# Kernel tuning notes

Measured on AMD Instinct MI355X. Metric: run time of the kernel, lower is better.

Reference implementation:

```python
import jax, jax.numpy as jnp
import numpy as np

N = 100000   # nodes
E = 1600000  # edges (avg degree 16)
F_IN = 128
HID = 128
C_OUT = 10
BN_EPS = 1e-5


def setup_inputs() -> dict:
    key = jax.random.key(0)
    ks = jax.random.split(key, 20)
    x = jax.random.normal(ks[0], (N, F_IN), jnp.float32)
    src = jax.random.randint(ks[1], (E,), 0, N)
    dst = jax.random.randint(ks[2], (E,), 0, N)
    def lin(k, fi, fo):
        return jax.random.normal(k, (fi, fo), jnp.float32) * (1.0 / np.sqrt(fi))
    inp = {
        "x": x, "src": src, "dst": dst,
        "W1": lin(ks[3], F_IN, HID), "b1": jnp.zeros((HID,), jnp.float32),
        "g1": jax.random.normal(ks[4], (HID,), jnp.float32) * 0.1 + 1.0,
        "be1": jax.random.normal(ks[5], (HID,), jnp.float32) * 0.1,
        "m1": jax.random.normal(ks[6], (HID,), jnp.float32) * 0.1,
        "v1": jax.random.uniform(ks[7], (HID,), jnp.float32, 0.5, 1.5),
        "W2": lin(ks[8], HID, HID), "b2": jnp.zeros((HID,), jnp.float32),
        "g2": jax.random.normal(ks[9], (HID,), jnp.float32) * 0.1 + 1.0,
        "be2": jax.random.normal(ks[10], (HID,), jnp.float32) * 0.1,
        "m2": jax.random.normal(ks[11], (HID,), jnp.float32) * 0.1,
        "v2": jax.random.uniform(ks[12], (HID,), jnp.float32, 0.5, 1.5),
        "W3": lin(ks[13], HID, C_OUT), "b3": jnp.zeros((C_OUT,), jnp.float32),
    }
    return inp


def _gcn_conv(x, W, b, src, dst):
    # PyG GCNConv: linear, add self-loops, symmetric deg^-1/2 normalization, scatter-add.
    h = x @ W                                            # [N, out]
    deg = jax.ops.segment_sum(jnp.ones((E,), h.dtype), dst, num_segments=N) + 1.0  # self-loop
    dinv = jax.lax.rsqrt(deg)                            # deg^{-1/2}, [N]
    coef = dinv[src] * dinv[dst]                         # per-edge norm, [E]
    agg = jax.ops.segment_sum(h[src] * coef[:, None], dst, num_segments=N)
    agg = agg + h * (dinv * dinv)[:, None]               # self-loop contribution
    return agg + b


def _bn_eval(x, g, be, m, v):
    return (x - m) * jax.lax.rsqrt(v + BN_EPS) * g + be


def reference(x, src, dst, W1, b1, g1, be1, m1, v1,
              W2, b2, g2, be2, m2, v2, W3, b3):
    h = jax.nn.relu(_bn_eval(_gcn_conv(x, W1, b1, src, dst), g1, be1, m1, v1))
    h = jax.nn.relu(_bn_eval(_gcn_conv(h, W2, b2, src, dst), g2, be2, m2, v2))
    return _gcn_conv(h, W3, b3, src, dst)                # [N, C_OUT] logits
```

## Files before the change

### kernel.cpp

```cpp
#include <hip/hip_runtime.h>

#define NN 100000
#define NE 1600000
#define FD 128
#define CO 10
#define BN_EPS 1e-5f
#define NBUK 782
#define NBUKP 784
#define BCAP 3072
#define SEGE 8192
#define NSEG 196
#define H3P 16

typedef __attribute__((ext_vector_type(8))) short short8;
typedef __attribute__((ext_vector_type(4))) float f32x4;

__device__ __forceinline__ unsigned short f2bf(float f) {
  unsigned int u = __builtin_bit_cast(unsigned int, f);
  u = (u + 0x7FFFu + ((u >> 16) & 1u)) >> 16;
  return (unsigned short)u;
}
__device__ __forceinline__ float bf2f(unsigned short h) {
  unsigned int u = ((unsigned int)h) << 16;
  return __builtin_bit_cast(float, u);
}
__device__ __forceinline__ float blo(unsigned int u) {
  return __builtin_bit_cast(float, u << 16);
}
__device__ __forceinline__ float bhi(unsigned int u) {
  return __builtin_bit_cast(float, u & 0xFFFF0000u);
}
__device__ __forceinline__ unsigned int cvt_pk_bf16(float a, float b) {
  unsigned int r;
  asm("v_cvt_pk_bf16_f32 %0, %1, %2" : "=v"(r) : "v"(a), "v"(b));
  return r;
}

__global__ __launch_bounds__(256) void k_hist_prep(
    const int* __restrict__ dst, int* __restrict__ histM,
    const float* __restrict__ W1, const float* __restrict__ W2,
    unsigned short* __restrict__ w1hi, unsigned short* __restrict__ w1lo,
    unsigned short* __restrict__ w2hi, unsigned short* __restrict__ w2lo,
    const float* __restrict__ b1, const float* __restrict__ g1,
    const float* __restrict__ be1, const float* __restrict__ m1,
    const float* __restrict__ v1,
    const float* __restrict__ b2, const float* __restrict__ g2,
    const float* __restrict__ be2, const float* __restrict__ m2,
    const float* __restrict__ v2,
    float* __restrict__ sc1, float* __restrict__ sh1,
    float* __restrict__ sc2, float* __restrict__ sh2) {
  __shared__ int hist[NBUK];
  int b = blockIdx.x, t = threadIdx.x;
  if (b < NSEG) {
    for (int i = t; i < NBUK; i += 256) hist[i] = 0;
    __syncthreads();
    int e0 = b * SEGE, e1 = min(e0 + SEGE, NE);
    for (int e = e0 + t; e < e1; e += 256) atomicAdd(&hist[dst[e] >> 7], 1);
    __syncthreads();
    for (int i = t; i < NBUK; i += 256) histM[b * NBUKP + i] = hist[i];
  } else if (b < NSEG + 128) {
    int bb = b - NSEG;
    const float* W = (bb < 64) ? W1 : W2;
    unsigned short* whi = (bb < 64) ? w1hi : w2hi;
    unsigned short* wlo = (bb < 64) ? w1lo : w2lo;
    int i = (bb & 63) * 256 + t;
    int k = i >> 7, n = i & 127;
    float w = W[i];
    unsigned short h = f2bf(w);
    unsigned short l = f2bf(w - bf2f(h));
    int idx = ((((k >> 5) * 8) + (n >> 4)) * 64 + ((k >> 3) & 3) * 16 + (n & 15)) * 8 + (k & 7);
    whi[idx] = h;
    wlo[idx] = l;
  } else {
    if (t < FD) {
      float s = g1[t] * rsqrtf(v1[t] + BN_EPS);
      sc1[t] = s;
      sh1[t] = (b1[t] - m1[t]) * s + be1[t];
    } else if (t < 2 * FD) {
      int f = t - FD;
      float s = g2[f] * rsqrtf(v2[f] + BN_EPS);
      sc2[f] = s;
      sh2[f] = (b2[f] - m2[f]) * s + be2[f];
    }
  }
}

__global__ __launch_bounds__(256) void k_colscan(const int* __restrict__ histM,
                                                 int* __restrict__ segbase,
                                                 int* __restrict__ btot) {
  __shared__ int lds[256];
  int b = blockIdx.x, t = threadIdx.x;
  int v = (t < NSEG) ? histM[t * NBUKP + b] : 0;
  lds[t] = v;
  __syncthreads();
  int mine = v;
  for (int off = 1; off < 256; off <<= 1) {
    int add = (t >= off) ? lds[t - off] : 0;
    __syncthreads();
    lds[t] += add;
    __syncthreads();
  }
  if (t < NSEG) segbase[t * NBUKP + b] = lds[t] - mine;
  if (t == 255) btot[b] = lds[255];
}

__global__ __launch_bounds__(256) void k_scatter2(const int* __restrict__ src,
                                                  const int* __restrict__ dst,
                                                  const int* __restrict__ segbase,
                                                  unsigned int* __restrict__ buck) {
  __shared__ int base[NBUK];
  int b = blockIdx.x, t = threadIdx.x;
  for (int i = t; i < NBUK; i += 256) base[i] = segbase[b * NBUKP + i];
  __syncthreads();
  int e0 = b * SEGE, e1 = min(e0 + SEGE, NE);
  for (int e = e0 + t; e < e1; e += 256) {
    int s = src[e], d = dst[e];
    int bk = d >> 7;
    int slot = atomicAdd(&base[bk], 1);
    buck[(size_t)bk * BCAP + slot] = ((unsigned int)(d & 127) << 17) | (unsigned int)s;
  }
}

__global__ __launch_bounds__(256) void k_finalize(const int* __restrict__ btot,
                                                  const unsigned int* __restrict__ buck,
                                                  uint4* __restrict__ nrange,
                                                  int* __restrict__ csr_src) {
  __shared__ unsigned int ebuf[BCAP];
  __shared__ int cnt[128];
  __shared__ int xoff[128];
  int b = blockIdx.x, t = threadIdx.x;
  int nb = btot[b];
  const unsigned int* bp = buck + (size_t)b * BCAP;
  for (int i = t; i < nb; i += 256) ebuf[i] = bp[i];
  if (t < 128) cnt[t] = 0;
  __syncthreads();
  for (int i = t; i < nb; i += 256) atomicAdd(&cnt[ebuf[i] >> 17], 1);
  __syncthreads();
  if (t < 128) xoff[t] = cnt[t];
  __syncthreads();
  for (int off = 1; off < 128; off <<= 1) {
    int add = 0;
    if (t < 128 && t >= off) add = xoff[t - off];
    __syncthreads();
    if (t < 128) xoff[t] += add;
    __syncthreads();
  }
  if (t < 128) {
    int node = b * 128 + t;
    int ex = xoff[t] - cnt[t];
    if (node < NN) {
      uint4 nr;
      nr.x = (unsigned)(b * BCAP + ex);
      nr.y = (unsigned)cnt[t];
      nr.z = __builtin_bit_cast(unsigned int, rsqrtf((float)cnt[t] + 1.0f));
      nr.w = 0;
      nrange[node] = nr;
    }
    xoff[t] = ex;
    cnt[t] = 0;
  }
  __syncthreads();
  int base = b * BCAP;
  for (int i = t; i < nb; i += 256) {
    unsigned int p = ebuf[i];
    int dl = (int)(p >> 17);
    int l = atomicAdd(&cnt[dl], 1);
    csr_src[base + xoff[dl] + l] = (int)(p & 0x1FFFFu);
  }
}

__global__ __launch_bounds__(256) void k_gemm128_mfma(const float* __restrict__ X,
                                                      const unsigned short* __restrict__ whi,
                                                      const unsigned short* __restrict__ wlo,
                                                      const uint4* __restrict__ nrange,
                                                      unsigned short* __restrict__ Hbs,
                                                      int nrows) {
  int tid = threadIdx.x;
  int lane = tid & 63, wv = tid >> 6;
  int lg = lane >> 4, li = lane & 15;
  int wr0 = blockIdx.x * 64 + wv * 16;
  int row = wr0 + li;
  bool ok = row < nrows;

  short8 ahi[4], alo[4];
#pragma unroll
  for (int ks = 0; ks < 4; ++ks) {
    if (ok) {
      const float* xp = X + (unsigned)(row * FD + ks * 32 + lg * 8);
      float4 v0 = *(const float4*)xp;
      float4 v1 = *(const float4*)(xp + 4);
      float f[8] = {v0.x, v0.y, v0.z, v0.w, v1.x, v1.y, v1.z, v1.w};
      unsigned int hp[4], lp[4];
#pragma unroll
      for (int j = 0; j < 4; ++j) {
        float a = f[2 * j], c = f[2 * j + 1];
        hp[j] = cvt_pk_bf16(a, c);
        float ra = a - blo(hp[j]);
        float rc = c - bhi(hp[j]);
        lp[j] = cvt_pk_bf16(ra, rc);
      }
      uint4 hv = {hp[0], hp[1], hp[2], hp[3]};
      uint4 lv = {lp[0], lp[1], lp[2], lp[3]};
      ahi[ks] = __builtin_bit_cast(short8, hv);
      alo[ks] = __builtin_bit_cast(short8, lv);
    } else {
#pragma unroll
      for (int j = 0; j < 8; ++j) { ahi[ks][j] = 0; alo[ks][j] = 0; }
    }
  }

  int rb = wr0 + lg * 4;
  float dvr[4];
#pragma unroll
  for (int r = 0; r < 4; ++r)
    dvr[r] = (rb + r < nrows) ? __builtin_bit_cast(float, nrange[rb + r].z) : 0.f;

#pragma unroll
  for (int nt = 0; nt < 8; ++nt) {
    f32x4 acc = {0.f, 0.f, 0.f, 0.f};
#pragma unroll
    for (int ks = 0; ks < 4; ++ks) {
      unsigned int bidx = (unsigned)(((ks * 8 + nt) * 64 + lane) * 8);
      short8 bh = *(const short8*)&whi[bidx];
      short8 bl = *(const short8*)&wlo[bidx];
      acc = __builtin_amdgcn_mfma_f32_16x16x32_bf16(ahi[ks], bh, acc, 0, 0, 0);
      acc = __builtin_amdgcn_mfma_f32_16x16x32_bf16(alo[ks], bh, acc, 0, 0, 0);
      acc = __builtin_amdgcn_mfma_f32_16x16x32_bf16(ahi[ks], bl, acc, 0, 0, 0);
    }
    int col = nt * 16 + li;
#pragma unroll
    for (int r = 0; r < 4; ++r) {
      if (rb + r < nrows)
        Hbs[(unsigned)((rb + r) * FD + col)] = f2bf(acc[r] * dvr[r]);
    }
  }
}

__global__ __launch_bounds__(256) void k_gemm128_bf16A(const unsigned short* __restrict__ Ab,
                                                       const unsigned short* __restrict__ whi,
                                                       const unsigned short* __restrict__ wlo,
                                                       const uint4* __restrict__ nrange,
                                                       unsigned short* __restrict__ Hbs,
                                                       int nrows) {
  int tid = threadIdx.x;
  int lane = tid & 63, wv = tid >> 6;
  int lg = lane >> 4, li = lane & 15;
  int wr0 = blockIdx.x * 64 + wv * 16;
  int row = wr0 + li;
  bool ok = row < nrows;

  short8 ahi[4];
#pragma unroll
  for (int ks = 0; ks < 4; ++ks) {
    if (ok) {
      ahi[ks] = *(const short8*)(Ab + (unsigned)(row * FD + ks * 32 + lg * 8));
    } else {
#pragma unroll
      for (int j = 0; j < 8; ++j) ahi[ks][j] = 0;
    }
  }

  int rb = wr0 + lg * 4;
  float dvr[4];
#pragma unroll
  for (int r = 0; r < 4; ++r)
    dvr[r] = (rb + r < nrows) ? __builtin_bit_cast(float, nrange[rb + r].z) : 0.f;

#pragma unroll
  for (int nt = 0; nt < 8; ++nt) {
    f32x4 acc = {0.f, 0.f, 0.f, 0.f};
#pragma unroll
    for (int ks = 0; ks < 4; ++ks) {
      unsigned int bidx = (unsigned)(((ks * 8 + nt) * 64 + lane) * 8);
      short8 bh = *(const short8*)&whi[bidx];
      short8 bl = *(const short8*)&wlo[bidx];
      acc = __builtin_amdgcn_mfma_f32_16x16x32_bf16(ahi[ks], bh, acc, 0, 0, 0);
      acc = __builtin_amdgcn_mfma_f32_16x16x32_bf16(ahi[ks], bl, acc, 0, 0, 0);
    }
    int col = nt * 16 + li;
#pragma unroll
    for (int r = 0; r < 4; ++r) {
      if (rb + r < nrows)
        Hbs[(unsigned)((rb + r) * FD + col)] = f2bf(acc[r] * dvr[r]);
    }
  }
}

__global__ __launch_bounds__(256) void k_gather128(const uint4* __restrict__ nrange,
                                                   const int* __restrict__ csr_src,
                                                   const unsigned short* __restrict__ Hbs,
                                                   const float* __restrict__ sc,
                                                   const float* __restrict__ sh,
                                                   unsigned int* __restrict__ AGGb) {
  int node = blockIdx.x * 4 + (threadIdx.x >> 6);
  node = __builtin_amdgcn_readfirstlane(node);
  int lane = threadIdx.x & 63;
  const unsigned int* Hc = (const unsigned int*)Hbs;
  uint4 nr = nrange[node];
  int beg = (int)nr.x, end = (int)(nr.x + nr.y);
  float dv = __builtin_bit_cast(float, nr.z);
  float px0, px1 = 0.f, px2 = 0.f, px3 = 0.f;
  float py0, py1 = 0.f, py2 = 0.f, py3 = 0.f;
  {
    unsigned int us = Hc[(unsigned)(node * 64) + lane];
    px0 = blo(us); py0 = bhi(us);
  }
  int e = beg;
  for (; e + 3 < end; e += 4) {
    unsigned int u0 = Hc[((unsigned)csr_src[e + 0] << 6) + lane];
    unsigned int u1 = Hc[((unsigned)csr_src[e + 1] << 6) + lane];
    unsigned int u2 = Hc[((unsigned)csr_src[e + 2] << 6) + lane];
    unsigned int u3 = Hc[((unsigned)csr_src[e + 3] << 6) + lane];
    px0 += blo(u0); py0 += bhi(u0);
    px1 += blo(u1); py1 += bhi(u1);
    px2 += blo(u2); py2 += bhi(u2);
    px3 += blo(u3); py3 += bhi(u3);
  }
  for (; e < end; ++e) {
    unsigned int u0 = Hc[((unsigned)csr_src[e] << 6) + lane];
    px0 += blo(u0); py0 += bhi(u0);
  }
  float accx = ((px0 + px1) + (px2 + px3)) * dv;
  float accy = ((py0 + py1) + (py2 + py3)) * dv;
  float scx = sc[lane * 2], scy = sc[lane * 2 + 1];
  float shx = sh[lane * 2], shy = sh[lane * 2 + 1];
  accx = fmaxf(fmaf(accx, scx, shx), 0.f);
  accy = fmaxf(fmaf(accy, scy, shy), 0.f);
  AGGb[(unsigned)(node * 64) + lane] = cvt_pk_bf16(accx, accy);
}

__global__ __launch_bounds__(256) void k_gather128_out(const uint4* __restrict__ nrange,
                                                       const int* __restrict__ csr_src,
                                                       const unsigned short* __restrict__ Hbs,
                                                       const float* __restrict__ sc,
                                                       const float* __restrict__ sh,
                                                       const float* __restrict__ W3,
                                                       float* __restrict__ H3s) {
  int node = blockIdx.x * 4 + (threadIdx.x >> 6);
  node = __builtin_amdgcn_readfirstlane(node);
  int lane = threadIdx.x & 63;
  float w3r[20];
  {
    const float* wp = W3 + lane * 2 * CO;
#pragma unroll
    for (int j = 0; j < 20; ++j) w3r[j] = wp[j];
  }
  const unsigned int* Hc = (const unsigned int*)Hbs;
  uint4 nr = nrange[node];
  int beg = (int)nr.x, end = (int)(nr.x + nr.y);
  float dv = __builtin_bit_cast(float, nr.z);
  float px0, px1 = 0.f, px2 = 0.f, px3 = 0.f;
  float py0, py1 = 0.f, py2 = 0.f, py3 = 0.f;
  {
    unsigned int us = Hc[(unsigned)(node * 64) + lane];
    px0 = blo(us); py0 = bhi(us);
  }
  int e = beg;
  for (; e + 3 < end; e += 4) {
    unsigned int u0 = Hc[((unsigned)csr_src[e + 0] << 6) + lane];
    unsigned int u1 = Hc[((unsigned)csr_src[e + 1] << 6) + lane];
    unsigned int u2 = Hc[((unsigned)csr_src[e + 2] << 6) + lane];
    unsigned int u3 = Hc[((unsigned)csr_src[e + 3] << 6) + lane];
    px0 += blo(u0); py0 += bhi(u0);
    px1 += blo(u1); py1 += bhi(u1);
    px2 += blo(u2); py2 += bhi(u2);
    px3 += blo(u3); py3 += bhi(u3);
  }
  for (; e < end; ++e) {
    unsigned int u0 = Hc[((unsigned)csr_src[e] << 6) + lane];
    px0 += blo(u0); py0 += bhi(u0);
  }
  float accx = ((px0 + px1) + (px2 + px3)) * dv;
  float accy = ((py0 + py1) + (py2 + py3)) * dv;
  float scx = sc[lane * 2], scy = sc[lane * 2 + 1];
  float shx = sh[lane * 2], shy = sh[lane * 2 + 1];
  accx = fmaxf(fmaf(accx, scx, shx), 0.f);
  accy = fmaxf(fmaf(accy, scy, shy), 0.f);
  float p[10];
#pragma unroll
  for (int c = 0; c < CO; ++c) p[c] = fmaf(accx, w3r[c], accy * w3r[10 + c]);
#pragma unroll
  for (int off = 32; off >= 1; off >>= 1) {
#pragma unroll
    for (int c = 0; c < CO; ++c) p[c] += __shfl_xor(p[c], off);
  }
#pragma unroll
  for (int c = 0; c < CO; ++c)
    if (lane == c) H3s[(unsigned)(node * H3P + c)] = p[c] * dv;
}

__global__ __launch_bounds__(256) void k_gather10(const uint4* __restrict__ nrange,
                                                  const int* __restrict__ csr_src,
                                                  const float* __restrict__ H3s,
                                                  const float* __restrict__ b3,
                                                  float* __restrict__ out) {
  int node = blockIdx.x * 16 + (threadIdx.x >> 4);
  if (node >= NN) return;
  int c = threadIdx.x & 15;
  uint4 nr = nrange[node];
  int beg = (int)nr.x, end = (int)(nr.x + nr.y);
  float dv = __builtin_bit_cast(float, nr.z);
  float acc = 0.f;
  if (c < CO) acc = H3s[(unsigned)(node * H3P + c)];
  for (int e = beg; e < end; ++e) {
    int s = csr_src[e];
    if (c < CO) acc += H3s[(unsigned)(s * H3P + c)];
  }
  if (c < CO) out[(unsigned)(node * CO + c)] = fmaf(acc, dv, b3[c]);
}

extern "C" void kernel_launch(void* const* d_in, const int* in_sizes, int n_in,
                              void* d_out, int out_size, void* d_ws, size_t ws_size,
                              hipStream_t stream) {
  const float* x = (const float*)d_in[0];
  const int* src = (const int*)d_in[1];
  const int* dst = (const int*)d_in[2];
  const float* W1 = (const float*)d_in[3];
  const float* b1 = (const float*)d_in[4];
  const float* g1 = (const float*)d_in[5];
  const float* be1 = (const float*)d_in[6];
  const float* m1 = (const float*)d_in[7];
  const float* v1 = (const float*)d_in[8];
  const float* W2 = (const float*)d_in[9];
  const float* b2 = (const float*)d_in[10];
  const float* g2 = (const float*)d_in[11];
  const float* be2 = (const float*)d_in[12];
  const float* m2 = (const float*)d_in[13];
  const float* v2 = (const float*)d_in[14];
  const float* W3 = (const float*)d_in[15];
  const float* b3 = (const float*)d_in[16];
  float* out = (float*)d_out;

  char* wsb = (char*)d_ws;
  int* histM = (int*)wsb;                      wsb += (size_t)NSEG * NBUKP * 4;
  int* segbase = (int*)wsb;                    wsb += (size_t)NSEG * NBUKP * 4;
  int* btot = (int*)wsb;                       wsb += NBUKP * 4;
  uint4* nrange = (uint4*)wsb;                 wsb += (size_t)NN * 16;
  float* sc1 = (float*)wsb;                    wsb += FD * 4;
  float* sh1 = (float*)wsb;                    wsb += FD * 4;
  float* sc2 = (float*)wsb;                    wsb += FD * 4;
  float* sh2 = (float*)wsb;                    wsb += FD * 4;
  unsigned short* w1hi = (unsigned short*)wsb; wsb += FD * FD * 2;
  unsigned short* w1lo = (unsigned short*)wsb; wsb += FD * FD * 2;
  unsigned short* w2hi = (unsigned short*)wsb; wsb += FD * FD * 2;
  unsigned short* w2lo = (unsigned short*)wsb; wsb += FD * FD * 2;
  int* csr_src = (int*)wsb;                    wsb += (size_t)NBUK * BCAP * 4;
  unsigned int* buck = (unsigned int*)wsb;     wsb += (size_t)NBUK * BCAP * 4;
  unsigned int* AGGb = (unsigned int*)wsb;     wsb += (size_t)NN * FD * 2;
  unsigned short* Hbs = (unsigned short*)wsb;  wsb += (size_t)NN * FD * 2;
  float* H3s = (float*)wsb;                    wsb += (size_t)NN * H3P * 4;

  k_hist_prep<<<NSEG + 129, 256, 0, stream>>>(dst, histM, W1, W2,
                                              w1hi, w1lo, w2hi, w2lo,
                                              b1, g1, be1, m1, v1,
                                              b2, g2, be2, m2, v2,
                                              sc1, sh1, sc2, sh2);
  k_colscan<<<NBUK, 256, 0, stream>>>(histM, segbase, btot);
  k_scatter2<<<NSEG, 256, 0, stream>>>(src, dst, segbase, buck);
  k_finalize<<<NBUK, 256, 0, stream>>>(btot, buck, nrange, csr_src);

  int gemm_blocks = (NN + 63) / 64;
  int gat_blocks = (NN + 3) / 4;

  k_gemm128_mfma<<<gemm_blocks, 256, 0, stream>>>(x, w1hi, w1lo, nrange, Hbs, NN);
  k_gather128<<<gat_blocks, 256, 0, stream>>>(nrange, csr_src, Hbs, sc1, sh1, AGGb);
  k_gemm128_bf16A<<<gemm_blocks, 256, 0, stream>>>((const unsigned short*)AGGb,
                                                   w2hi, w2lo, nrange, Hbs, NN);
  k_gather128_out<<<gat_blocks, 256, 0, stream>>>(nrange, csr_src, Hbs, sc2, sh2, W3, H3s);
  k_gather10<<<(NN + 15) / 16, 256, 0, stream>>>(nrange, csr_src, H3s, b3, out);
}
```

Before: 310.7 us.

## Fuse layer-1 gather/BN/ReLU into layer-2 GEMM via LDS staging

Replaces the separate layer-1 neighbour-gather kernel and the bf16 GEMM kernel with one kernel. Each wave gathers 16 nodes' aggregated rows, applies BN and ReLU, stages them in shared memory, then feeds them straight into the MFMA GEMM. This removes the intermediate AGGb round trip through global memory and one kernel launch. In exchange the gather runs with 16 serial nodes per wave and only 1563 blocks, which lowers the parallelism available to hide gather latency.

```diff
diff --git a/kernel.cpp b/kernel.cpp
--- a/kernel.cpp
+++ b/kernel.cpp
@@ -11,6 +11,7 @@
 #define SEGE 8192
 #define NSEG 196
 #define H3P 16
+#define RPAD 68
 
 typedef __attribute__((ext_vector_type(8))) short short8;
 typedef __attribute__((ext_vector_type(4))) float f32x4;
@@ -236,35 +237,74 @@
   }
 }
 
-__global__ __launch_bounds__(256) void k_gemm128_bf16A(const unsigned short* __restrict__ Ab,
-                                                       const unsigned short* __restrict__ whi,
-                                                       const unsigned short* __restrict__ wlo,
-                                                       const uint4* __restrict__ nrange,
-                                                       unsigned short* __restrict__ Hbs,
-                                                       int nrows) {
+__global__ __launch_bounds__(256) void k_gather_gemm(const uint4* __restrict__ nrange,
+                                                     const int* __restrict__ csr_src,
+                                                     const unsigned short* __restrict__ Hbs,
+                                                     const float* __restrict__ sc,
+                                                     const float* __restrict__ sh,
+                                                     const unsigned short* __restrict__ whi,
+                                                     const unsigned short* __restrict__ wlo,
+                                                     unsigned short* __restrict__ Hbs2) {
+  __shared__ unsigned int rows[4][16][RPAD];
   int tid = threadIdx.x;
   int lane = tid & 63, wv = tid >> 6;
   int lg = lane >> 4, li = lane & 15;
-  int wr0 = blockIdx.x * 64 + wv * 16;
-  int row = wr0 + li;
-  bool ok = row < nrows;
+  int n0 = blockIdx.x * 64 + wv * 16;
+  const unsigned int* Hc = (const unsigned int*)Hbs;
+  float scx = sc[lane * 2], scy = sc[lane * 2 + 1];
+  float shx = sh[lane * 2], shy = sh[lane * 2 + 1];
+
+  for (int r16 = 0; r16 < 16; ++r16) {
+    int node = __builtin_amdgcn_readfirstlane(n0 + r16);
+    unsigned int uo = 0;
+    if (node < NN) {
+      uint4 nr = nrange[node];
+      int beg = (int)nr.x, end = (int)(nr.x + nr.y);
+      float dv = __builtin_bit_cast(float, nr.z);
+      float px0, px1 = 0.f, px2 = 0.f, px3 = 0.f;
+      float py0, py1 = 0.f, py2 = 0.f, py3 = 0.f;
+      {
+        unsigned int us = Hc[(unsigned)(node * 64) + lane];
+        px0 = blo(us); py0 = bhi(us);
+      }
+      int e = beg;
+      for (; e + 3 < end; e += 4) {
+        unsigned int u0 = Hc[((unsigned)csr_src[e + 0] << 6) + lane];
+        unsigned int u1 = Hc[((unsigned)csr_src[e + 1] << 6) + lane];
+        unsigned int u2 = Hc[((unsigned)csr_src[e + 2] << 6) + lane];
+        unsigned int u3 = Hc[((unsigned)csr_src[e + 3] << 6) + lane];
+        px0 += blo(u0); py0 += bhi(u0);
+        px1 += blo(u1); py1 += bhi(u1);
+        px2 += blo(u2); py2 += bhi(u2);
+        px3 += blo(u3); py3 += bhi(u3);
+      }
+      for (; e < end; ++e) {
+        unsigned int u0 = Hc[((unsigned)csr_src[e] << 6) + lane];
+        px0 += blo(u0); py0 += bhi(u0);
+      }
+      float accx = ((px0 + px1) + (px2 + px3)) * dv;
+      float accy = ((py0 + py1) + (py2 + py3)) * dv;
+      accx = fmaxf(fmaf(accx, scx, shx), 0.f);
+      accy = fmaxf(fmaf(accy, scy, shy), 0.f);
+      uo = cvt_pk_bf16(accx, accy);
+    }
+    rows[wv][r16][lane] = uo;
+  }
 
   short8 ahi[4];
-#pragma unroll
-  for (int ks = 0; ks < 4; ++ks) {
-    if (ok) {
-      ahi[ks] = *(const short8*)(Ab + (unsigned)(row * FD + ks * 32 + lg * 8));
-    } else {
-#pragma unroll
-      for (int j = 0; j < 8; ++j) ahi[ks][j] = 0;
-    }
-  }
-
-  int rb = wr0 + lg * 4;
+  {
+    const unsigned int* rp = &rows[wv][li][0];
+#pragma unroll
+    for (int ks = 0; ks < 4; ++ks) {
+      uint4 q = *(const uint4*)(rp + ks * 16 + lg * 4);
+      ahi[ks] = __builtin_bit_cast(short8, q);
+    }
+  }
+  int rb = n0 + lg * 4;
   float dvr[4];
 #pragma unroll
   for (int r = 0; r < 4; ++r)
-    dvr[r] = (rb + r < nrows) ? __builtin_bit_cast(float, nrange[rb + r].z) : 0.f;
+    dvr[r] = (rb + r < NN) ? __builtin_bit_cast(float, nrange[rb + r].z) : 0.f;
 
 #pragma unroll
   for (int nt = 0; nt < 8; ++nt) {
@@ -280,53 +320,10 @@
     int col = nt * 16 + li;
 #pragma unroll
     for (int r = 0; r < 4; ++r) {
-      if (rb + r < nrows)
-        Hbs[(unsigned)((rb + r) * FD + col)] = f2bf(acc[r] * dvr[r]);
-    }
-  }
-}
-
-__global__ __launch_bounds__(256) void k_gather128(const uint4* __restrict__ nrange,
-                                                   const int* __restrict__ csr_src,
-                                                   const unsigned short* __restrict__ Hbs,
-                                                   const float* __restrict__ sc,
-                                                   const float* __restrict__ sh,
-                                                   unsigned int* __restrict__ AGGb) {
-  int node = blockIdx.x * 4 + (threadIdx.x >> 6);
-  node = __builtin_amdgcn_readfirstlane(node);
-  int lane = threadIdx.x & 63;
-  const unsigned int* Hc = (const unsigned int*)Hbs;
-  uint4 nr = nrange[node];
-  int beg = (int)nr.x, end = (int)(nr.x + nr.y);
-  float dv = __builtin_bit_cast(float, nr.z);
-  float px0, px1 = 0.f, px2 = 0.f, px3 = 0.f;
-  float py0, py1 = 0.f, py2 = 0.f, py3 = 0.f;
-  {
-    unsigned int us = Hc[(unsigned)(node * 64) + lane];
-    px0 = blo(us); py0 = bhi(us);
-  }
-  int e = beg;
-  for (; e + 3 < end; e += 4) {
-    unsigned int u0 = Hc[((unsigned)csr_src[e + 0] << 6) + lane];
-    unsigned int u1 = Hc[((unsigned)csr_src[e + 1] << 6) + lane];
-    unsigned int u2 = Hc[((unsigned)csr_src[e + 2] << 6) + lane];
-    unsigned int u3 = Hc[((unsigned)csr_src[e + 3] << 6) + lane];
-    px0 += blo(u0); py0 += bhi(u0);
-    px1 += blo(u1); py1 += bhi(u1);
-    px2 += blo(u2); py2 += bhi(u2);
-    px3 += blo(u3); py3 += bhi(u3);
-  }
-  for (; e < end; ++e) {
-    unsigned int u0 = Hc[((unsigned)csr_src[e] << 6) + lane];
-    px0 += blo(u0); py0 += bhi(u0);
-  }
-  float accx = ((px0 + px1) + (px2 + px3)) * dv;
-  float accy = ((py0 + py1) + (py2 + py3)) * dv;
-  float scx = sc[lane * 2], scy = sc[lane * 2 + 1];
-  float shx = sh[lane * 2], shy = sh[lane * 2 + 1];
-  accx = fmaxf(fmaf(accx, scx, shx), 0.f);
-  accy = fmaxf(fmaf(accy, scy, shy), 0.f);
-  AGGb[(unsigned)(node * 64) + lane] = cvt_pk_bf16(accx, accy);
+      if (rb + r < NN)
+        Hbs2[(unsigned)((rb + r) * FD + col)] = f2bf(acc[r] * dvr[r]);
+    }
+  }
 }
 
 __global__ __launch_bounds__(256) void k_gather128_out(const uint4* __restrict__ nrange,
@@ -446,8 +443,8 @@
   unsigned short* w2lo = (unsigned short*)wsb; wsb += FD * FD * 2;
   int* csr_src = (int*)wsb;                    wsb += (size_t)NBUK * BCAP * 4;
   unsigned int* buck = (unsigned int*)wsb;     wsb += (size_t)NBUK * BCAP * 4;
-  unsigned int* AGGb = (unsigned int*)wsb;     wsb += (size_t)NN * FD * 2;
-  unsigned short* Hbs = (unsigned short*)wsb;  wsb += (size_t)NN * FD * 2;
+  unsigned short* Hbs1 = (unsigned short*)wsb; wsb += (size_t)NN * FD * 2;
+  unsigned short* Hbs2 = (unsigned short*)wsb; wsb += (size_t)NN * FD * 2;
   float* H3s = (float*)wsb;                    wsb += (size_t)NN * H3P * 4;
 
   k_hist_prep<<<NSEG + 129, 256, 0, stream>>>(dst, histM, W1, W2,
@@ -460,12 +457,11 @@
   k_finalize<<<NBUK, 256, 0, stream>>>(btot, buck, nrange, csr_src);
 
   int gemm_blocks = (NN + 63) / 64;
-  int gat_blocks = (NN + 3) / 4;
-
-  k_gemm128_mfma<<<gemm_blocks, 256, 0, stream>>>(x, w1hi, w1lo, nrange, Hbs, NN);
-  k_gather128<<<gat_blocks, 256, 0, stream>>>(nrange, csr_src, Hbs, sc1, sh1, AGGb);
-  k_gemm128_bf16A<<<gemm_blocks, 256, 0, stream>>>((const unsigned short*)AGGb,
-                                                   w2hi, w2lo, nrange, Hbs, NN);
-  k_gather128_out<<<gat_blocks, 256, 0, stream>>>(nrange, csr_src, Hbs, sc2, sh2, W3, H3s);
+
+  k_gemm128_mfma<<<gemm_blocks, 256, 0, stream>>>(x, w1hi, w1lo, nrange, Hbs1, NN);
+  k_gather_gemm<<<gemm_blocks, 256, 0, stream>>>(nrange, csr_src, Hbs1, sc1, sh1,
+                                                 w2hi, w2lo, Hbs2);
+  k_gather128_out<<<(NN + 3) / 4, 256, 0, stream>>>(nrange, csr_src, Hbs2,
+                                                    sc2, sh2, W3, H3s);
   k_gather10<<<(NN + 15) / 16, 256, 0, stream>>>(nrange, csr_src, H3s, b3, out);
 }
```

New measurement: 310.8 us. No clear change (+0.1%).
